# Kernel optimization log

Measured on AMD Instinct MI355X. Metric: run time of the kernel, lower is better.

Reference implementation:

```python
import jax, jax.numpy as jnp
import numpy as np

N, D_IN, UNITS = 8192, 2048, 2048


def setup_inputs() -> dict:
    key = jax.random.key(0)
    ks = jax.random.split(key, 14)
    s_in = 1.0 / np.sqrt(D_IN)
    s_u = 1.0 / np.sqrt(UNITS)
    return {
        "x": jax.random.normal(ks[0], (N, UNITS), jnp.float32),
        "y": jax.random.normal(ks[1], (N, D_IN), jnp.float32),
        # W* act on y (D_IN -> UNITS), U* act on x (UNITS -> UNITS)
        "Wz": jax.random.normal(ks[2], (D_IN, UNITS), jnp.float32) * s_in,
        "bz": jnp.zeros((UNITS,), jnp.float32),
        "Uz": jax.random.normal(ks[3], (UNITS, UNITS), jnp.float32) * s_u,
        "buz": jax.random.normal(ks[4], (UNITS,), jnp.float32) * 0.05,  # glorot-init bias
        "Wr": jax.random.normal(ks[5], (D_IN, UNITS), jnp.float32) * s_in,
        "br": jnp.zeros((UNITS,), jnp.float32),
        "Ur": jax.random.normal(ks[6], (UNITS, UNITS), jnp.float32) * s_u,
        "bur": jnp.zeros((UNITS,), jnp.float32),
        "Wg": jax.random.normal(ks[7], (D_IN, UNITS), jnp.float32) * s_in,
        "bg": jax.random.normal(ks[8], (UNITS,), jnp.float32) * 0.05,  # glorot-init bias
        "Ug": jax.random.normal(ks[9], (UNITS, UNITS), jnp.float32) * s_u,
        "bug": jnp.zeros((UNITS,), jnp.float32),
    }


def reference(x, y, Wz, bz, Uz, buz, Wr, br, Ur, bur, Wg, bg, Ug, bug):
    # Batch the three y-projections and the two x-projections into single GEMMs.
    Wy = y @ jnp.concatenate([Wz, Wr, Wg], axis=1)          # [N, 3*UNITS]
    Ux = x @ jnp.concatenate([Uz, Ur], axis=1)               # [N, 2*UNITS]
    u = Wz.shape[1]
    z = Wy[:, :u] + bz + Ux[:, :u] + buz                     # NOTE: no sigmoid (faithful to source)
    r = Wy[:, u:2 * u] + br + Ux[:, u:] + bur                # NOTE: no sigmoid (faithful to source)
    h = jnp.tanh(Wy[:, 2 * u:] + bg + (r * x) @ Ug + bug)
    return (1.0 - z) * x + z * h
```

## Files before the change

### kernel.cpp

```cpp
#include <hip/hip_runtime.h>
#include <hip/hip_bf16.h>
#include <cstdint>
#include <cmath>

typedef __bf16 bf16;
typedef __bf16 bf16x8 __attribute__((ext_vector_type(8)));
typedef __bf16 bf16x4 __attribute__((ext_vector_type(4)));
typedef float f32x4 __attribute__((ext_vector_type(4)));

#define NROWS 8192
#define UNITS 2048
#define NT 64
#define NSPLIT 32

__device__ __forceinline__ void gload_lds16(const bf16* g, const bf16* lds) {
  __builtin_amdgcn_global_load_lds(
      (const __attribute__((address_space(1))) uint32_t*)(uintptr_t)g,
      (__attribute__((address_space(3))) uint32_t*)(uint32_t)(uintptr_t)lds,
      16, 0, 0);
}

#define BARR do { asm volatile("" ::: "memory"); __builtin_amdgcn_s_barrier(); \
                  asm volatile("" ::: "memory"); } while (0)
#define WAITV(N) asm volatile("s_waitcnt vmcnt(" #N ")" ::: "memory")

__device__ __forceinline__ float fast_tanh(float v) {
  float e = __expf(2.f * v);
  return 1.f - 2.f / (e + 1.f);
}

__global__ void pack_xy_kernel(const float* __restrict__ x, const float* __restrict__ y,
                               bf16* __restrict__ xb, bf16* __restrict__ yb) {
  size_t n4 = (size_t)NROWS * UNITS / 4;
  size_t stride = (size_t)gridDim.x * blockDim.x;
  for (size_t i = (size_t)blockIdx.x * blockDim.x + threadIdx.x; i < n4; i += stride) {
    float4 vx = ((const float4*)x)[i];
    float4 vy = ((const float4*)y)[i];
    bf16x4 ox = {(bf16)vx.x, (bf16)vx.y, (bf16)vx.z, (bf16)vx.w};
    bf16x4 oy = {(bf16)vy.x, (bf16)vy.y, (bf16)vy.z, (bf16)vy.w};
    ((bf16x4*)xb)[i] = ox;
    ((bf16x4*)yb)[i] = oy;
  }
}

__global__ void transpose_cvt6_kernel(const float* __restrict__ Wz, const float* __restrict__ Uz,
                                      const float* __restrict__ Wr, const float* __restrict__ Ur,
                                      const float* __restrict__ Wg, const float* __restrict__ Ug,
                                      bf16* __restrict__ Bzr, bf16* __restrict__ Bgt) {
  __shared__ float t[32][33];
  const float* src;
  bf16* dst;
  int koff;
  switch (blockIdx.z) {
    case 0: src = Wz; dst = Bzr;                         koff = 0;    break;
    case 1: src = Uz; dst = Bzr;                         koff = 2048; break;
    case 2: src = Wr; dst = Bzr + (size_t)2048 * 4096;   koff = 0;    break;
    case 3: src = Ur; dst = Bzr + (size_t)2048 * 4096;   koff = 2048; break;
    case 4: src = Wg; dst = Bgt;                         koff = 0;    break;
    default: src = Ug; dst = Bgt;                        koff = 2048; break;
  }
  int j0 = blockIdx.x * 32, k0 = blockIdx.y * 32;
  int tx = threadIdx.x & 31, ty = threadIdx.x >> 5;
#pragma unroll
  for (int i = 0; i < 32; i += 8)
    t[ty + i][tx] = src[(size_t)(k0 + ty + i) * UNITS + j0 + tx];
  __syncthreads();
#pragma unroll
  for (int i = 0; i < 32; i += 8)
    dst[(size_t)(j0 + ty + i) * 4096 + koff + k0 + tx] = (bf16)t[tx][ty + i];
}

template <int EPI>
__global__ __launch_bounds__(512, 2)
void gemm256(const bf16* __restrict__ A0, const bf16* __restrict__ A1,
             const bf16* __restrict__ Bt,
             const float* __restrict__ bias_a, const float* __restrict__ bias_b,
             const float* __restrict__ bias_c, const float* __restrict__ bias_d,
             const bf16* __restrict__ xin, bf16* __restrict__ zbuf,
             bf16* __restrict__ rxbuf, float* __restrict__ outbuf) {
  __shared__ bf16 LDS[2][32768];
  const int tid = threadIdx.x;
  const int wv = tid >> 6, lane = tid & 63;
  const int wr = wv >> 2, wc = wv & 3;

  const int nl = (int)gridDim.x >> 3;
  const int xc = (int)blockIdx.x & 7;
  const int l = (int)blockIdx.x >> 3;
  const int bxq = nl >> 4;
  const int by = (xc & 1) * 16 + (l & 15);
  const int bx = (xc >> 1) * bxq + (l >> 4);
  const int brow = by * 256;
  const int bcol = bx * 256;

  const int rr = lane >> 2;
  const int kk_st = ((lane & 3) * 8) ^ ((rr & 6) << 2);
  int offA[2][2], offB[2][2], dstA[2][2], dstB[2][2];
#pragma unroll
  for (int H = 0; H < 2; ++H)
#pragma unroll
    for (int c = 0; c < 2; ++c) {
      int ssA = H * 8 + wv;
      offA[H][c] = (brow + c * 128 + (ssA >> 1) * 16 + rr) * 2048 + (ssA & 1) * 32 + kk_st;
      dstA[H][c] = c * 8192 + ssA * 512;
      int ssB = (wv >> 2) * 8 + H * 4 + (wv & 3);
      offB[H][c] = (bcol + c * 128 + (ssB >> 1) * 16 + rr) * 4096 + (ssB & 1) * 32 + kk_st;
      dstB[H][c] = 16384 + c * 8192 + ssB * 512;
    }

  const int lr = lane & 15;
  const int kread = ((lane >> 4) * 8) ^ ((lr & 6) << 2);
  const int abase = wr * 8192 + lr * 32 + kread;
  const int bbase = 16384 + (wc >> 1) * 8192 + (wc & 1) * 4096 + lr * 32 + kread;

#define ST_A(TI, H, BUF)                                                      \
  if ((TI) < NT) {                                                            \
    const bf16* _s = ((TI) < NSPLIT) ? A0 + (size_t)(TI)*64                   \
                                     : A1 + (size_t)((TI)-NSPLIT) * 64;       \
    gload_lds16(_s + offA[H][0], (BUF) + dstA[H][0]);                         \
    gload_lds16(_s + offA[H][1], (BUF) + dstA[H][1]);                         \
  }
#define ST_B(TI, H, BUF)                                                      \
  if ((TI) < NT) {                                                            \
    const bf16* _s = Bt + (size_t)(TI)*64;                                    \
    gload_lds16(_s + offB[H][0], (BUF) + dstB[H][0]);                         \
    gload_lds16(_s + offB[H][1], (BUF) + dstB[H][1]);                         \
  }
#define RD_B(DST, LP, NB)                                                     \
  _Pragma("unroll") for (int kh = 0; kh < 2; ++kh)                            \
  _Pragma("unroll") for (int n = 0; n < 2; ++n)                               \
      DST[n][kh] = *(const bf16x8*)((LP) + bbase + ((n + 2 * (NB)) * 2 + kh) * 512);
#define RD_A(DST, LP, MB)                                                     \
  _Pragma("unroll") for (int kh = 0; kh < 2; ++kh)                            \
  _Pragma("unroll") for (int m = 0; m < 4; ++m)                               \
      DST[m][kh] = *(const bf16x8*)((LP) + abase + ((m + 4 * (MB)) * 2 + kh) * 512);
#define MFMA_Q(AARR, BARR_, MOFF, NOFF)                                       \
  __builtin_amdgcn_s_setprio(1);                                              \
  _Pragma("unroll") for (int kh = 0; kh < 2; ++kh)                            \
  _Pragma("unroll") for (int m = 0; m < 4; ++m)                               \
  _Pragma("unroll") for (int n = 0; n < 2; ++n)                               \
      acc[m + MOFF][n + NOFF] = __builtin_amdgcn_mfma_f32_16x16x32_bf16(      \
          AARR[m][kh], BARR_[n][kh], acc[m + MOFF][n + NOFF], 0, 0, 0);       \
  __builtin_amdgcn_s_setprio(0);

  f32x4 acc[8][4];
#pragma unroll
  for (int m = 0; m < 8; ++m)
#pragma unroll
    for (int n = 0; n < 4; ++n) {
      f32x4 zz = {0.f, 0.f, 0.f, 0.f};
      acc[m][n] = zz;
    }

  bf16x8 a0[4][2], a1[4][2], b0[2][2], b1[2][2];

  {
    bf16* L0 = &LDS[0][0];
    bf16* L1 = &LDS[1][0];
    ST_A(0, 0, L0); ST_B(0, 0, L0); ST_A(0, 1, L0); ST_B(0, 1, L0);
    ST_B(1, 0, L1); ST_A(1, 0, L1);
    WAITV(4);
    BARR;
    RD_B(b0, L0, 0);
  }

#define TILE(T, CUR, NXT, W3, W4)                                             \
  {                                                                           \
    const bf16* Lc = &LDS[CUR][0];                                            \
    bf16* Lcw = &LDS[CUR][0];                                                 \
    const bf16* Ln = &LDS[NXT][0];                                            \
    bf16* Lnw = &LDS[NXT][0];                                                 \
                                                                      \
    ST_A((T) + 1, 1, Lnw);                                                    \
    RD_A(a0, Lc, 0);                                                          \
    BARR;                                                                     \
    MFMA_Q(a0, b0, 0, 0);                                                     \
    BARR;                                                                     \
                                                                      \
    ST_B((T) + 1, 1, Lnw);                                                    \
    RD_A(a1, Lc, 1);                                                          \
    BARR;                                                                     \
    MFMA_Q(a1, b0, 4, 0);                                                     \
    BARR;                                                                     \
                                                                      \
    ST_B((T) + 2, 0, Lcw);                                                    \
    RD_B(b1, Lc, 1);                                                          \
    BARR;                                                                     \
    MFMA_Q(a0, b1, 0, 2);                                                     \
    WAITV(W3); BARR;                                                          \
                                                                      \
    ST_A((T) + 2, 0, Lcw);                                                    \
    if ((T) + 1 < NT) { RD_B(b0, Ln, 0); }                                    \
    BARR;                                                                     \
    MFMA_Q(a1, b1, 4, 2);                                                     \
    WAITV(W4); BARR;                                                          \
  }

#pragma unroll 1
  for (int t = 0; t < NT - 2; t += 2) {
    TILE(t, 0, 1, 8, 4);
    TILE(t + 1, 1, 0, 8, 4);
  }
  TILE(NT - 2, 0, 1, 6, 0);
  TILE(NT - 1, 1, 0, 0, 0);

  const int lq = (lane >> 4) << 2;
  const int lc = lane & 15;
  const int rowb = brow + wr * 128;
  const int colb = bcol + wc * 64;
  if constexpr (EPI == 0) {
    if (bcol < UNITS) {
#pragma unroll
      for (int m = 0; m < 8; ++m)
#pragma unroll
        for (int n = 0; n < 4; ++n) {
          int col = colb + n * 16 + lc;
          float ba = bias_a[col] + bias_b[col];
#pragma unroll
          for (int q = 0; q < 4; ++q) {
            int row = rowb + m * 16 + lq + q;
            zbuf[(size_t)row * UNITS + col] = (bf16)(acc[m][n][q] + ba);
          }
        }
    } else {
#pragma unroll
      for (int m = 0; m < 8; ++m)
#pragma unroll
        for (int n = 0; n < 4; ++n) {
          int col = colb - UNITS + n * 16 + lc;
          float bc = bias_c[col] + bias_d[col];
#pragma unroll
          for (int q = 0; q < 4; ++q) {
            int row = rowb + m * 16 + lq + q;
            size_t idx = (size_t)row * UNITS + col;
            float r = acc[m][n][q] + bc;
            rxbuf[idx] = (bf16)(r * (float)xin[idx]);
          }
        }
    }
  } else {
#pragma unroll
    for (int m = 0; m < 8; ++m)
#pragma unroll
      for (int n = 0; n < 4; ++n) {
        int col = colb + n * 16 + lc;
        float bg_ = bias_a[col] + bias_b[col];
#pragma unroll
        for (int q = 0; q < 4; ++q) {
          int row = rowb + m * 16 + lq + q;
          size_t idx = (size_t)row * UNITS + col;
          float h = fast_tanh(acc[m][n][q] + bg_);
          float zv = (float)zbuf[idx];
          float xv = (float)xin[idx];
          outbuf[idx] = (1.f - zv) * xv + zv * h;
        }
      }
  }
#undef ST_A
#undef ST_B
#undef RD_A
#undef RD_B
#undef MFMA_Q
#undef TILE
}

extern "C" void kernel_launch(void* const* d_in, const int* in_sizes, int n_in,
                              void* d_out, int out_size, void* d_ws, size_t ws_size,
                              hipStream_t stream) {
  const float* x   = (const float*)d_in[0];
  const float* y   = (const float*)d_in[1];
  const float* Wz  = (const float*)d_in[2];
  const float* bz  = (const float*)d_in[3];
  const float* Uz  = (const float*)d_in[4];
  const float* buz = (const float*)d_in[5];
  const float* Wr  = (const float*)d_in[6];
  const float* br  = (const float*)d_in[7];
  const float* Ur  = (const float*)d_in[8];
  const float* bur = (const float*)d_in[9];
  const float* Wg  = (const float*)d_in[10];
  const float* bg  = (const float*)d_in[11];
  const float* Ug  = (const float*)d_in[12];
  const float* bug = (const float*)d_in[13];
  float* out = (float*)d_out;

  char* w = (char*)d_ws;
  bf16* Ybf = (bf16*)w;  w += (size_t)NROWS * UNITS * 2;
  bf16* Xbf = (bf16*)w;  w += (size_t)NROWS * UNITS * 2;
  bf16* RX  = (bf16*)w;  w += (size_t)NROWS * UNITS * 2;
  bf16* Bzr = (bf16*)w;  w += (size_t)4096 * 4096 * 2;
  bf16* Bgt = (bf16*)w;  w += (size_t)2048 * 4096 * 2;
  bf16* Zb  = (bf16*)w;  w += (size_t)NROWS * UNITS * 2;

  pack_xy_kernel<<<2048, 256, 0, stream>>>(x, y, Xbf, Ybf);
  dim3 tg(64, 64, 6);
  transpose_cvt6_kernel<<<tg, 256, 0, stream>>>(Wz, Uz, Wr, Ur, Wg, Ug, Bzr, Bgt);

  gemm256<0><<<512, 512, 0, stream>>>(Ybf, Xbf, Bzr, bz, buz, br, bur, Xbf, Zb, RX, nullptr);
  gemm256<1><<<256, 512, 0, stream>>>(Ybf, RX, Bgt, bg, bug, nullptr, nullptr, Xbf, Zb, nullptr, out);
}
```

Baseline: 451.6 us.

## Load B operand directly from global into registers, bypassing LDS

The B operand tiles no longer go through LDS. Each wave loads its own B fragments straight from global memory into registers, which halves the LDS footprint and pipeline. The intent is to cut LDS traffic and memory use, which may raise occupancy and drop the B ds_reads. The cost is that B data shared across waves is now fetched redundantly from global/L2, and the vmcnt wait counts and the loop tail were retuned in a way that risks ordering errors.

```diff
diff --git a/kernel.cpp b/kernel.cpp
--- a/kernel.cpp
+++ b/kernel.cpp
@@ -23,6 +23,7 @@
 #define BARR do { asm volatile("" ::: "memory"); __builtin_amdgcn_s_barrier(); \
                   asm volatile("" ::: "memory"); } while (0)
 #define WAITV(N) asm volatile("s_waitcnt vmcnt(" #N ")" ::: "memory")
+#define FENCE asm volatile("" ::: "memory")
 
 __device__ __forceinline__ float fast_tanh(float v) {
   float e = __expf(2.f * v);
@@ -78,7 +79,7 @@
              const float* __restrict__ bias_c, const float* __restrict__ bias_d,
              const bf16* __restrict__ xin, bf16* __restrict__ zbuf,
              bf16* __restrict__ rxbuf, float* __restrict__ outbuf) {
-  __shared__ bf16 LDS[2][32768];
+  __shared__ bf16 LDS[2][16384];
   const int tid = threadIdx.x;
   const int wv = tid >> 6, lane = tid & 63;
   const int wr = wv >> 2, wc = wv & 3;
@@ -94,7 +95,7 @@
 
   const int rr = lane >> 2;
   const int kk_st = ((lane & 3) * 8) ^ ((rr & 6) << 2);
-  int offA[2][2], offB[2][2], dstA[2][2], dstB[2][2];
+  int offA[2][2], dstA[2][2];
 #pragma unroll
   for (int H = 0; H < 2; ++H)
 #pragma unroll
@@ -102,15 +103,17 @@
       int ssA = H * 8 + wv;
       offA[H][c] = (brow + c * 128 + (ssA >> 1) * 16 + rr) * 2048 + (ssA & 1) * 32 + kk_st;
       dstA[H][c] = c * 8192 + ssA * 512;
-      int ssB = (wv >> 2) * 8 + H * 4 + (wv & 3);
-      offB[H][c] = (bcol + c * 128 + (ssB >> 1) * 16 + rr) * 4096 + (ssB & 1) * 32 + kk_st;
-      dstB[H][c] = 16384 + c * 8192 + ssB * 512;
     }
 
   const int lr = lane & 15;
   const int kread = ((lane >> 4) * 8) ^ ((lr & 6) << 2);
   const int abase = wr * 8192 + lr * 32 + kread;
-  const int bbase = 16384 + (wc >> 1) * 8192 + (wc & 1) * 4096 + lr * 32 + kread;
+
+  const int colbase = bcol + (wc >> 1) * 128 + (wc & 1) * 64;
+  const bf16* gB[4];
+#pragma unroll
+  for (int i = 0; i < 4; ++i)
+    gB[i] = Bt + (size_t)(colbase + i * 16 + lr) * 4096 + ((lane >> 4) * 8);
 
 #define ST_A(TI, H, BUF)                                                      \
   if ((TI) < NT) {                                                            \
@@ -119,16 +122,10 @@
     gload_lds16(_s + offA[H][0], (BUF) + dstA[H][0]);                         \
     gload_lds16(_s + offA[H][1], (BUF) + dstA[H][1]);                         \
   }
-#define ST_B(TI, H, BUF)                                                      \
-  if ((TI) < NT) {                                                            \
-    const bf16* _s = Bt + (size_t)(TI)*64;                                    \
-    gload_lds16(_s + offB[H][0], (BUF) + dstB[H][0]);                         \
-    gload_lds16(_s + offB[H][1], (BUF) + dstB[H][1]);                         \
-  }
-#define RD_B(DST, LP, NB)                                                     \
+#define GLD_B(DST, NB, T)                                                     \
+  _Pragma("unroll") for (int n = 0; n < 2; ++n)                               \
   _Pragma("unroll") for (int kh = 0; kh < 2; ++kh)                            \
-  _Pragma("unroll") for (int n = 0; n < 2; ++n)                               \
-      DST[n][kh] = *(const bf16x8*)((LP) + bbase + ((n + 2 * (NB)) * 2 + kh) * 512);
+      DST[n][kh] = *(const bf16x8*)(gB[(NB)*2 + n] + (size_t)(T)*64 + kh * 32);
 #define RD_A(DST, LP, MB)                                                     \
   _Pragma("unroll") for (int kh = 0; kh < 2; ++kh)                            \
   _Pragma("unroll") for (int m = 0; m < 4; ++m)                               \
@@ -156,52 +153,51 @@
   {
     bf16* L0 = &LDS[0][0];
     bf16* L1 = &LDS[1][0];
-    ST_A(0, 0, L0); ST_B(0, 0, L0); ST_A(0, 1, L0); ST_B(0, 1, L0);
-    ST_B(1, 0, L1); ST_A(1, 0, L1);
-    WAITV(4);
+    ST_A(0, 0, L0); FENCE;
+    ST_A(0, 1, L0); FENCE;
+    GLD_B(b0, 0, 0); FENCE;
+    ST_A(1, 0, L1); FENCE;
+    GLD_B(b1, 1, 0);
+    WAITV(12);
     BARR;
-    RD_B(b0, L0, 0);
-  }
-
-#define TILE(T, CUR, NXT, W3, W4)                                             \
+  }
+
+#define TILE(T, CUR, NXT, W1, W3)                                             \
   {                                                                           \
     const bf16* Lc = &LDS[CUR][0];                                            \
     bf16* Lcw = &LDS[CUR][0];                                                 \
-    const bf16* Ln = &LDS[NXT][0];                                            \
     bf16* Lnw = &LDS[NXT][0];                                                 \
                                                                       \
+    RD_A(a0, Lc, 0);                                                          \
+    WAITV(W1);                                                                \
+    BARR;                                                                     \
+    MFMA_Q(a0, b0, 0, 0);                                                     \
+    BARR;                                                                     \
+                                                                      \
+    RD_A(a1, Lc, 1);                                                          \
     ST_A((T) + 1, 1, Lnw);                                                    \
-    RD_A(a0, Lc, 0);                                                          \
-    BARR;                                                                     \
-    MFMA_Q(a0, b0, 0, 0);                                                     \
+    BARR;                                                                     \
+    MFMA_Q(a1, b0, 4, 0);                                                     \
     BARR;                                                                     \
                                                                       \
-    ST_B((T) + 1, 1, Lnw);                                                    \
-    RD_A(a1, Lc, 1);                                                          \
-    BARR;                                                                     \
-    MFMA_Q(a1, b0, 4, 0);                                                     \
-    BARR;                                                                     \
-                                                                      \
-    ST_B((T) + 2, 0, Lcw);                                                    \
-    RD_B(b1, Lc, 1);                                                          \
+    WAITV(W3);                                                                \
+    if ((T) + 1 < NT) { GLD_B(b0, 0, (T) + 1); }                              \
+    FENCE;                                                                    \
+    ST_A((T) + 2, 0, Lcw);                                                    \
     BARR;                                                                     \
     MFMA_Q(a0, b1, 0, 2);                                                     \
-    WAITV(W3); BARR;                                                          \
-                                                                      \
-    ST_A((T) + 2, 0, Lcw);                                                    \
-    if ((T) + 1 < NT) { RD_B(b0, Ln, 0); }                                    \
-    BARR;                                                                     \
     MFMA_Q(a1, b1, 4, 2);                                                     \
-    WAITV(W4); BARR;                                                          \
+    FENCE;                                                                    \
+    if ((T) + 1 < NT) { GLD_B(b1, 1, (T) + 1); }                              \
+    BARR;                                                                     \
   }
 
 #pragma unroll 1
-  for (int t = 0; t < NT - 2; t += 2) {
-    TILE(t, 0, 1, 8, 4);
-    TILE(t + 1, 1, 0, 8, 4);
-  }
-  TILE(NT - 2, 0, 1, 6, 0);
-  TILE(NT - 1, 1, 0, 0, 0);
+  for (int t = 0; t < NT - 1; t += 2) {
+    TILE(t, 0, 1, 6, 2);
+    if (t + 1 < NT - 1) { TILE(t + 1, 1, 0, 6, 2); }
+  }
+  TILE(NT - 1, 1, 0, 4, 0);
 
   const int lq = (lane >> 4) << 2;
   const int lc = lane & 15;
@@ -256,9 +252,8 @@
       }
   }
 #undef ST_A
-#undef ST_B
+#undef GLD_B
 #undef RD_A
-#undef RD_B
 #undef MFMA_Q
 #undef TILE
 }
```

After: 642.1 us. +42.2%, slower.

## Halve GEMM main-loop barrier phases and vectorize transpose-convert stores

Applied to the files above, without the earlier changes.

The GEMM tile loop drops from four barrier-separated phases to two. Each phase now issues both global-to-LDS stores and the A/B fragment reads before running two MFMA quarters, with a single vmcnt wait at the end of the tile. The aim is to cut barrier and synchronisation overhead, at the cost of coarser interleaving between memory traffic and MFMA work and more registers live at once. Separately, the weight transpose/convert kernel now processes 64-row k tiles and writes packed bf16x2 values, giving wider stores and half as many blocks.

```diff
diff --git a/kernel.cpp b/kernel.cpp
--- a/kernel.cpp
+++ b/kernel.cpp
@@ -6,6 +6,7 @@
 typedef __bf16 bf16;
 typedef __bf16 bf16x8 __attribute__((ext_vector_type(8)));
 typedef __bf16 bf16x4 __attribute__((ext_vector_type(4)));
+typedef __bf16 bf16x2 __attribute__((ext_vector_type(2)));
 typedef float f32x4 __attribute__((ext_vector_type(4)));
 
 #define NROWS 8192
@@ -47,7 +48,7 @@
                                       const float* __restrict__ Wr, const float* __restrict__ Ur,
                                       const float* __restrict__ Wg, const float* __restrict__ Ug,
                                       bf16* __restrict__ Bzr, bf16* __restrict__ Bgt) {
-  __shared__ float t[32][33];
+  __shared__ float t[64][33];
   const float* src;
   bf16* dst;
   int koff;
@@ -59,15 +60,18 @@
     case 4: src = Wg; dst = Bgt;                         koff = 0;    break;
     default: src = Ug; dst = Bgt;                        koff = 2048; break;
   }
-  int j0 = blockIdx.x * 32, k0 = blockIdx.y * 32;
+  int j0 = blockIdx.x * 32, k0 = blockIdx.y * 64;
   int tx = threadIdx.x & 31, ty = threadIdx.x >> 5;
 #pragma unroll
-  for (int i = 0; i < 32; i += 8)
+  for (int i = 0; i < 64; i += 8)
     t[ty + i][tx] = src[(size_t)(k0 + ty + i) * UNITS + j0 + tx];
   __syncthreads();
 #pragma unroll
-  for (int i = 0; i < 32; i += 8)
-    dst[(size_t)(j0 + ty + i) * 4096 + koff + k0 + tx] = (bf16)t[tx][ty + i];
+  for (int i = 0; i < 32; i += 8) {
+    int j = j0 + ty + i;
+    bf16x2 v = {(bf16)t[2 * tx][ty + i], (bf16)t[2 * tx + 1][ty + i]};
+    *(bf16x2*)&dst[(size_t)j * 4096 + koff + k0 + 2 * tx] = v;
+  }
 }
 
 template <int EPI>
@@ -160,48 +164,40 @@
     ST_B(1, 0, L1); ST_A(1, 0, L1);
     WAITV(4);
     BARR;
-    RD_B(b0, L0, 0);
-  }
-
-#define TILE(T, CUR, NXT, W3, W4)                                             \
+  }
+
+#define TILE(T, CUR, NXT, WB)                                                 \
   {                                                                           \
     const bf16* Lc = &LDS[CUR][0];                                            \
     bf16* Lcw = &LDS[CUR][0];                                                 \
-    const bf16* Ln = &LDS[NXT][0];                                            \
     bf16* Lnw = &LDS[NXT][0];                                                 \
-                                                                      \
+                                                                     \
     ST_A((T) + 1, 1, Lnw);                                                    \
+    ST_B((T) + 1, 1, Lnw);                                                    \
     RD_A(a0, Lc, 0);                                                          \
+    RD_B(b0, Lc, 0);                                                          \
+    RD_B(b1, Lc, 1);                                                          \
     BARR;                                                                     \
     MFMA_Q(a0, b0, 0, 0);                                                     \
+    MFMA_Q(a0, b1, 0, 2);                                                     \
     BARR;                                                                     \
-                                                                      \
-    ST_B((T) + 1, 1, Lnw);                                                    \
+                                                                     \
+    ST_B((T) + 2, 0, Lcw);                                                    \
+    ST_A((T) + 2, 0, Lcw);                                                    \
     RD_A(a1, Lc, 1);                                                          \
     BARR;                                                                     \
     MFMA_Q(a1, b0, 4, 0);                                                     \
-    BARR;                                                                     \
-                                                                      \
-    ST_B((T) + 2, 0, Lcw);                                                    \
-    RD_B(b1, Lc, 1);                                                          \
-    BARR;                                                                     \
-    MFMA_Q(a0, b1, 0, 2);                                                     \
-    WAITV(W3); BARR;                                                          \
-                                                                      \
-    ST_A((T) + 2, 0, Lcw);                                                    \
-    if ((T) + 1 < NT) { RD_B(b0, Ln, 0); }                                    \
-    BARR;                                                                     \
     MFMA_Q(a1, b1, 4, 2);                                                     \
-    WAITV(W4); BARR;                                                          \
+    WAITV(WB); BARR;                                                          \
   }
 
 #pragma unroll 1
   for (int t = 0; t < NT - 2; t += 2) {
-    TILE(t, 0, 1, 8, 4);
-    TILE(t + 1, 1, 0, 8, 4);
-  }
-  TILE(NT - 2, 0, 1, 6, 0);
-  TILE(NT - 1, 1, 0, 0, 0);
+    TILE(t, 0, 1, 4);
+    TILE(t + 1, 1, 0, 4);
+  }
+  TILE(NT - 2, 0, 1, 0);
+  TILE(NT - 1, 1, 0, 0);
 
   const int lq = (lane >> 4) << 2;
   const int lc = lane & 15;
@@ -291,7 +287,7 @@
   bf16* Zb  = (bf16*)w;  w += (size_t)NROWS * UNITS * 2;
 
   pack_xy_kernel<<<2048, 256, 0, stream>>>(x, y, Xbf, Ybf);
-  dim3 tg(64, 64, 6);
+  dim3 tg(64, 32, 6);
   transpose_cvt6_kernel<<<tg, 256, 0, stream>>>(Wz, Uz, Wr, Ur, Wg, Ug, Bzr, Bgt);
 
   gemm256<0><<<512, 512, 0, stream>>>(Ybf, Xbf, Bzr, bz, buz, br, bur, Xbf, Zb, RX, nullptr);
```

Result: faster. 426.9 us (-5.5%).
